# Kernel tuning notes

Measured on AMD Instinct MI355X. Metric: run time of the kernel, lower is better.

Reference implementation:

```python
import jax, jax.numpy as jnp
import numpy as np

NUM_HEADS = 8
NUM_GROUPS = 8
NUM_ITERATIONS = 3
DT = 0.1
EPS = 1e-5


def group_norm(x, scale, bias):
    # x: [B, C, H, W], GroupNorm(8, C)
    B, C, H, W = x.shape
    xg = x.reshape(B, NUM_GROUPS, C // NUM_GROUPS, H, W)
    mean = xg.mean(axis=(2, 3, 4), keepdims=True)
    var = xg.var(axis=(2, 3, 4), keepdims=True)
    xg = (xg - mean) * jax.lax.rsqrt(var + EPS)
    x = xg.reshape(B, C, H, W)
    return x * scale[None, :, None, None] + bias[None, :, None, None]


def setup_inputs() -> dict:
    key = jax.random.key(0)
    ks = jax.random.split(key, 4)
    B, C, H, W = 8, 512, 32, 32
    x = jax.random.normal(ks[0], (B, C, H, W), dtype=jnp.float32)
    qkv_w = jax.random.normal(ks[1], (3 * C, C), dtype=jnp.float32) * (1.0 / np.sqrt(C))
    proj_w = jax.random.normal(ks[2], (C, C), dtype=jnp.float32) * (1.0 / np.sqrt(C))
    inl_w = jax.random.normal(ks[3], (C, C), dtype=jnp.float32) * (1.0 / np.sqrt(C))
    return {
        "x": x,
        "gn_scale": jnp.ones((C,), jnp.float32),
        "gn_bias": jnp.zeros((C,), jnp.float32),
        "qkv_w": qkv_w,
        "qkv_b": jnp.zeros((3 * C,), jnp.float32),
        "proj_w": proj_w,
        "proj_b": jnp.zeros((C,), jnp.float32),
        "inl_w": inl_w,
        "inl_b": jnp.zeros((C,), jnp.float32),
    }


def reference(x, gn_scale, gn_bias, qkv_w, qkv_b, proj_w, proj_b, inl_w, inl_b):
    B, C, H, W = x.shape
    nh = NUM_HEADS
    hd = C // nh
    S = H * W

    h = group_norm(x, gn_scale, gn_bias)

    # 1x1 conv == channel matmul
    qkv = jnp.einsum('oc,bchw->bohw', qkv_w, h) + qkv_b[None, :, None, None]
    q, k, v = jnp.split(qkv, 3, axis=1)  # each [B, C, H, W]

    def to_heads(t):  # [B, C, H, W] -> [B, nh, S, hd]
        return t.reshape(B, nh, hd, S).transpose(0, 1, 3, 2)

    q, k, v = to_heads(q), to_heads(k), to_heads(v)

    scale = hd ** (-0.5)
    attn = jax.nn.softmax(jnp.einsum('bnsd,bntd->bnst', q, k) * scale, axis=-1)
    h = jnp.einsum('bnst,bntd->bnsd', attn, v)  # [B, nh, S, hd]

    # back to [B, S, C] for INL refinement
    h_flat = h.transpose(0, 1, 3, 2).reshape(B, C, S).transpose(0, 2, 1)

    # SimpleINLDynamics: iterative Euler refinement x <- x + dt * tanh(W x + b)
    def step(hf, _):
        hf = hf + DT * jnp.tanh(jnp.einsum('bsc,oc->bso', hf, inl_w) + inl_b)
        return hf, None
    h_flat, _ = jax.lax.scan(step, h_flat, None, length=NUM_ITERATIONS)

    h = h_flat.transpose(0, 2, 1).reshape(B, C, H, W)
    h = jnp.einsum('oc,bchw->bohw', proj_w, h) + proj_b[None, :, None, None]
    return x + h
```

## Files before the change

### kernel.cpp

```cpp
#include <hip/hip_runtime.h>
#include <math.h>

#define B_ 8
#define C_ 512
#define S_ 1024
#define HD 64
#define NHEADS 8
#define NGROUPS 8
#define DT_STEP 0.1f
#define EPS_GN 1e-5f
#define LOG2E 1.4426950408889634f

typedef __attribute__((ext_vector_type(8))) short bf16x8;
typedef __attribute__((ext_vector_type(4))) float f32x4;
typedef __attribute__((ext_vector_type(8))) unsigned short ushort8;
typedef __attribute__((ext_vector_type(4))) unsigned short ushort4_t;

static __device__ __forceinline__ unsigned short f2bf(float f) {
  unsigned int u = __builtin_bit_cast(unsigned int, f);
  u += 0x7fff + ((u >> 16) & 1);
  return (unsigned short)(u >> 16);
}

static __device__ __forceinline__ unsigned short f2bf_fast(float f) {
  unsigned int u = __builtin_bit_cast(unsigned int, f);
  return (unsigned short)((u + 0x8000u) >> 16);
}

static __device__ __forceinline__ float bf2f(unsigned short u) {
  unsigned int t = ((unsigned int)u) << 16;
  return __builtin_bit_cast(float, t);
}

static __device__ __forceinline__ float exp2_raw(float x) {
  return __builtin_amdgcn_exp2f(x);
}

static __device__ __forceinline__ float fast_tanh(float x) {
  float xc = fminf(fmaxf(x, -15.f), 15.f);
  float e = exp2_raw(xc * (2.0f * LOG2E));
  return (e - 1.f) / (e + 1.f);
}

__global__ __launch_bounds__(256) void prep_kernel(
    const float* __restrict__ a, const float* __restrict__ b, const float* __restrict__ c,
    unsigned short* __restrict__ A, unsigned short* __restrict__ B, unsigned short* __restrict__ C,
    const float* __restrict__ x, float* __restrict__ gpart) {
  int bid = blockIdx.x;
  int tid = threadIdx.x;
  if (bid < 384) {
    int off = bid * 2048;
    int i = off + tid * 8;
    f32x4 v0 = *(const f32x4*)(a + i);
    f32x4 v1 = *(const f32x4*)(a + i + 4);
    ushort8 o;
    o[0] = f2bf(v0[0]); o[1] = f2bf(v0[1]); o[2] = f2bf(v0[2]); o[3] = f2bf(v0[3]);
    o[4] = f2bf(v1[0]); o[5] = f2bf(v1[1]); o[6] = f2bf(v1[2]); o[7] = f2bf(v1[3]);
    *(ushort8*)(A + i) = o;
    return;
  }
  if (bid < 640) {
    const float* src; unsigned short* dst; int off;
    if (bid < 512) { src = b; dst = B; off = (bid - 384) * 2048; }
    else { src = c; dst = C; off = (bid - 512) * 2048; }
    int i = off + tid * 8;
    f32x4 v0 = *(const f32x4*)(src + i);
    f32x4 v1 = *(const f32x4*)(src + i + 4);
    ushort8 o;
    o[0] = f2bf(v0[0]); o[1] = f2bf(v0[1]); o[2] = f2bf(v0[2]); o[3] = f2bf(v0[3]);
    o[4] = f2bf(v1[0]); o[5] = f2bf(v1[1]); o[6] = f2bf(v1[2]); o[7] = f2bf(v1[3]);
    int orow = i >> 9, cbase = i & 511;
    int dsti = (cbase >> 5) * 16384 + orow * 32 + (cbase & 31);
    *(ushort8*)(dst + dsti) = o;
    return;
  }
  int sbid = bid - 640;
  int bg = sbid >> 3, chunk = sbid & 7;
  const float* xp = x + (size_t)bg * 65536 + (size_t)chunk * 8192;
  float sum = 0.f, sq = 0.f;
  #pragma unroll
  for (int i = 0; i < 8; ++i) {
    f32x4 v = *(const f32x4*)(xp + i * 1024 + tid * 4);
    sum += v[0] + v[1] + v[2] + v[3];
    sq += v[0]*v[0] + v[1]*v[1] + v[2]*v[2] + v[3]*v[3];
  }
  #pragma unroll
  for (int off = 32; off >= 1; off >>= 1) {
    sum += __shfl_xor(sum, off, 64);
    sq  += __shfl_xor(sq, off, 64);
  }
  __shared__ float s1[4], s2[4];
  int wave = tid >> 6, lane = tid & 63;
  if (lane == 0) { s1[wave] = sum; s2[wave] = sq; }
  __syncthreads();
  if (tid == 0) {
    float S = s1[0] + s1[1] + s1[2] + s1[3];
    float Q = s2[0] + s2[1] + s2[2] + s2[3];
    gpart[bg * 16 + chunk * 2] = S;
    gpart[bg * 16 + chunk * 2 + 1] = Q;
  }
}

__global__ __launch_bounds__(256) void gn_apply_t(
    const float* __restrict__ x, const float* __restrict__ gpart,
    const float* __restrict__ scale, const float* __restrict__ bias,
    unsigned short* __restrict__ h_t) {
  int bid = blockIdx.x;
  int bg = bid >> 4, st = bid & 15;
  int b = bg >> 3, g = bg & 7;
  float S = 0.f, Q = 0.f;
  #pragma unroll
  for (int i = 0; i < 8; ++i) {
    S += gpart[bg * 16 + i * 2];
    Q += gpart[bg * 16 + i * 2 + 1];
  }
  float mean = S / 65536.f;
  float var = Q / 65536.f - mean * mean;
  float inv = rsqrtf(var + EPS_GN);

  int tid = threadIdx.x;
  int sl = tid >> 2;
  int cq = (tid & 3) * 16;
  float sA[16], sB[16];
  #pragma unroll
  for (int u = 0; u < 16; ++u) {
    float scv = scale[g * 64 + cq + u];
    sA[u] = inv * scv;
    sB[u] = bias[g * 64 + cq + u] - mean * inv * scv;
  }

  const float* xp = x + ((size_t)b * C_ + (size_t)g * 64) * S_;
  __shared__ float tile[64][65];
  #pragma unroll
  for (int it = 0; it < 16; ++it) {
    int lin = it * 256 + tid;
    int c = lin >> 6, s = lin & 63;
    tile[c][s] = xp[(size_t)c * S_ + st * 64 + s];
  }
  __syncthreads();
  unsigned short vals[16];
  #pragma unroll
  for (int u = 0; u < 16; ++u)
    vals[u] = f2bf_fast(tile[cq + u][sl] * sA[u] + sB[u]);
  unsigned short* dst = h_t + ((size_t)b * S_ + st * 64 + sl) * C_ + g * 64 + cq;
  ushort8 lo, hi;
  #pragma unroll
  for (int u = 0; u < 8; ++u) { lo[u] = vals[u]; hi[u] = vals[u + 8]; }
  *(ushort8*)dst = lo;
  *(ushort8*)(dst + 8) = hi;
}

template<int MB, int NB, int WMG, int WNG>
__device__ __forceinline__ void gemm_nt_core(
    const unsigned short* __restrict__ Ab,
    const unsigned short* __restrict__ Bb,
    unsigned short* ldsA, unsigned short* ldsB,
    f32x4* acc) {
  constexpr int TI = (MB / WMG) / 16;
  constexpr int TJ = (NB / WNG) / 16;
  constexpr int NQA = MB * 4 / 256;
  constexpr int NQB = NB * 4 / 256;
  const int K = 512;
  const int tid = threadIdx.x;
  const int w = tid >> 6, lane = tid & 63, quad = lane >> 4, l15 = lane & 15;
  const int wm = (WNG == 1) ? w : ((WMG == 1) ? 0 : (w >> 1));
  const int wn = (WNG == 1) ? 0 : ((WMG == 1) ? w : (w & 1));

  ushort8 apf[NQA], bpf[NQB];
  #pragma unroll
  for (int q = 0; q < NQA; ++q) {
    int c = q * 256 + tid;
    apf[q] = *(const ushort8*)(Ab + (size_t)(c >> 2) * K + (c & 3) * 8);
  }
  #pragma unroll
  for (int q = 0; q < NQB; ++q) {
    int c = q * 256 + tid;
    bpf[q] = *(const ushort8*)(Bb + (size_t)(c >> 2) * K + (c & 3) * 8);
  }

  for (int k0 = 0; k0 < K; k0 += 32) {
    __syncthreads();
    #pragma unroll
    for (int q = 0; q < NQA; ++q) {
      int c = q * 256 + tid;
      *(ushort8*)(ldsA + c * 8) = apf[q];
    }
    #pragma unroll
    for (int q = 0; q < NQB; ++q) {
      int c = q * 256 + tid;
      *(ushort8*)(ldsB + c * 8) = bpf[q];
    }
    __syncthreads();
    if (k0 + 32 < K) {
      #pragma unroll
      for (int q = 0; q < NQA; ++q) {
        int c = q * 256 + tid;
        apf[q] = *(const ushort8*)(Ab + (size_t)(c >> 2) * K + k0 + 32 + (c & 3) * 8);
      }
      #pragma unroll
      for (int q = 0; q < NQB; ++q) {
        int c = q * 256 + tid;
        bpf[q] = *(const ushort8*)(Bb + (size_t)(c >> 2) * K + k0 + 32 + (c & 3) * 8);
      }
    }
    bf16x8 af[TI], bfr[TJ];
    #pragma unroll
    for (int i = 0; i < TI; ++i)
      af[i] = *(const bf16x8*)(ldsA + (wm * (MB / WMG) + i * 16 + l15) * 32 + quad * 8);
    #pragma unroll
    for (int j = 0; j < TJ; ++j)
      bfr[j] = *(const bf16x8*)(ldsB + (wn * (NB / WNG) + j * 16 + l15) * 32 + quad * 8);
    #pragma unroll
    for (int i = 0; i < TI; ++i)
      #pragma unroll
      for (int j = 0; j < TJ; ++j)
        acc[i * TJ + j] = __builtin_amdgcn_mfma_f32_16x16x32_bf16(af[i], bfr[j], acc[i * TJ + j], 0, 0, 0);
  }
}

__global__ __launch_bounds__(256) void gemm_qkv_mfma(
    const unsigned short* __restrict__ Wbf, const unsigned short* __restrict__ h_t,
    const float* __restrict__ bias,
    unsigned short* __restrict__ Qt, unsigned short* __restrict__ Kt,
    unsigned short* __restrict__ Vt) {
  __shared__ __align__(16) unsigned short ldsA[128 * 32];
  __shared__ __align__(16) unsigned short ldsB[128 * 32];
  int b = blockIdx.z;
  int bm = blockIdx.y * 128, bn = blockIdx.x * 128;
  f32x4 acc[16];
  #pragma unroll
  for (int t = 0; t < 16; ++t) acc[t] = (f32x4){0.f, 0.f, 0.f, 0.f};
  gemm_nt_core<128, 128, 2, 2>(Wbf + (size_t)bm * 512,
                               h_t + ((size_t)b * S_ + bn) * 512, ldsA, ldsB, acc);
  int tid = threadIdx.x, w = tid >> 6, lane = tid & 63, quad = lane >> 4, l15 = lane & 15;
  int wm = w >> 1, wn = w & 1;
  int tensor = bm >> 9;
  float qscale = (tensor == 0) ? 0.125f * LOG2E : 1.0f;
  #pragma unroll
  for (int i = 0; i < 4; ++i) {
    #pragma unroll
    for (int j = 0; j < 4; ++j) {
      int m0 = bm + wm * 64 + i * 16 + quad * 4;
      int ng = bn + wn * 64 + j * 16 + l15;
      f32x4 v = acc[i * 4 + j];
      if (tensor < 2) {
        int head = (m0 >> 6) & 7, d0 = m0 & 63;
        ushort4_t pk;
        #pragma unroll
        for (int r = 0; r < 4; ++r) pk[r] = f2bf((v[r] + bias[m0 + r]) * qscale);
        unsigned short* dst = (tensor ? Kt : Qt) +
            (((size_t)(b * 8 + head) * S_ + ng) * 64 + d0);
        *(ushort4_t*)dst = pk;
      } else {
        #pragma unroll
        for (int r = 0; r < 4; ++r)
          Vt[(size_t)b * (C_ * S_) + (size_t)(m0 - 1024 + r) * S_ + ng] = f2bf(v[r] + bias[m0 + r]);
      }
    }
  }
}

__global__ __launch_bounds__(256) void attn_mfma(
    const unsigned short* __restrict__ Qt,
    const unsigned short* __restrict__ Kt,
    const unsigned short* __restrict__ Vt,
    unsigned short* __restrict__ hflat_bf) {
  int tid = threadIdx.x, wave = tid >> 6, lane = tid & 63;
  int quad = lane >> 4, l15 = lane & 15;
  int bid = blockIdx.x;
  int bn = bid & 63, sblk = bid >> 6, b = bn >> 3, n = bn & 7;
  int s0w = sblk * 128 + wave * 32;

  __shared__ unsigned short k_lds[64][72];
  __shared__ unsigned short v_lds[64][72];
  __shared__ unsigned short p_lds[4][2][16][72];

  const unsigned short* Kb = Kt + ((size_t)(b * 8 + n)) * S_ * 64;
  const unsigned short* Vb = Vt + ((size_t)b * C_ + n * 64) * S_;

  bf16x8 qa[2][2];
  #pragma unroll
  for (int g = 0; g < 2; ++g) {
    const unsigned short* Qb = Qt + (((size_t)(b * 8 + n)) * S_ + s0w + g * 16 + l15) * 64;
    qa[g][0] = *(const bf16x8*)(Qb + quad * 8);
    qa[g][1] = *(const bf16x8*)(Qb + 32 + quad * 8);
  }

  bf16x8 ones;
  #pragma unroll
  for (int j = 0; j < 8; ++j) ones[j] = (short)0x3F80;

  f32x4 o_acc[2][4];
  f32x4 l_acc[2];
  #pragma unroll
  for (int g = 0; g < 2; ++g) {
    l_acc[g] = (f32x4){0.f, 0.f, 0.f, 0.f};
    #pragma unroll
    for (int dc = 0; dc < 4; ++dc) o_acc[g][dc] = (f32x4){0.f, 0.f, 0.f, 0.f};
  }

  int row0 = tid >> 3, c80 = (tid & 7) * 8;
  int row1 = (tid + 256) >> 3, c81 = c80;

  ushort8 kreg[2], vreg[2];
  kreg[0] = *(const ushort8*)(Kb + (size_t)row0 * 64 + c80);
  kreg[1] = *(const ushort8*)(Kb + (size_t)row1 * 64 + c81);
  vreg[0] = *(const ushort8*)(Vb + (size_t)row0 * S_ + c80);
  vreg[1] = *(const ushort8*)(Vb + (size_t)row1 * S_ + c81);

  for (int t0 = 0; t0 < S_; t0 += 64) {
    __syncthreads();
    *(ushort8*)&k_lds[row0][c80] = kreg[0];
    *(ushort8*)&k_lds[row1][c81] = kreg[1];
    *(ushort8*)&v_lds[row0][c80] = vreg[0];
    *(ushort8*)&v_lds[row1][c81] = vreg[1];
    __syncthreads();
    if (t0 + 64 < S_) {
      int t1 = t0 + 64;
      kreg[0] = *(const ushort8*)(Kb + (size_t)(t1 + row0) * 64 + c80);
      kreg[1] = *(const ushort8*)(Kb + (size_t)(t1 + row1) * 64 + c81);
      vreg[0] = *(const ushort8*)(Vb + (size_t)row0 * S_ + t1 + c80);
      vreg[1] = *(const ushort8*)(Vb + (size_t)row1 * S_ + t1 + c81);
    }

    f32x4 sc[2][4];
    #pragma unroll
    for (int tc = 0; tc < 4; ++tc) {
      bf16x8 kb0 = *(const bf16x8*)&k_lds[tc * 16 + l15][quad * 8];
      bf16x8 kb1 = *(const bf16x8*)&k_lds[tc * 16 + l15][32 + quad * 8];
      #pragma unroll
      for (int g = 0; g < 2; ++g) {
        f32x4 c = {0.f, 0.f, 0.f, 0.f};
        c = __builtin_amdgcn_mfma_f32_16x16x32_bf16(kb0, qa[g][0], c, 0, 0, 0);
        sc[g][tc] = __builtin_amdgcn_mfma_f32_16x16x32_bf16(kb1, qa[g][1], c, 0, 0, 0);
      }
    }

    #pragma unroll
    for (int g = 0; g < 2; ++g)
      #pragma unroll
      for (int tc = 0; tc < 4; ++tc) {
        ushort4_t p4;
        #pragma unroll
        for (int r = 0; r < 4; ++r) p4[r] = f2bf_fast(exp2_raw(sc[g][tc][r]));
        *(ushort4_t*)&p_lds[wave][g][l15][tc * 16 + quad * 4] = p4;
      }

    bf16x8 pa[2][2];
    #pragma unroll
    for (int g = 0; g < 2; ++g) {
      pa[g][0] = *(const bf16x8*)&p_lds[wave][g][l15][quad * 8];
      pa[g][1] = *(const bf16x8*)&p_lds[wave][g][l15][32 + quad * 8];
      l_acc[g] = __builtin_amdgcn_mfma_f32_16x16x32_bf16(pa[g][0], ones, l_acc[g], 0, 0, 0);
      l_acc[g] = __builtin_amdgcn_mfma_f32_16x16x32_bf16(pa[g][1], ones, l_acc[g], 0, 0, 0);
    }
    #pragma unroll
    for (int dc = 0; dc < 4; ++dc) {
      bf16x8 vb0 = *(const bf16x8*)&v_lds[dc * 16 + l15][quad * 8];
      bf16x8 vb1 = *(const bf16x8*)&v_lds[dc * 16 + l15][32 + quad * 8];
      #pragma unroll
      for (int g = 0; g < 2; ++g) {
        o_acc[g][dc] = __builtin_amdgcn_mfma_f32_16x16x32_bf16(pa[g][0], vb0, o_acc[g][dc], 0, 0, 0);
        o_acc[g][dc] = __builtin_amdgcn_mfma_f32_16x16x32_bf16(pa[g][1], vb1, o_acc[g][dc], 0, 0, 0);
      }
    }
  }

  #pragma unroll
  for (int g = 0; g < 2; ++g) {
    float inv_l[4];
    #pragma unroll
    for (int r = 0; r < 4; ++r) inv_l[r] = 1.f / l_acc[g][r];
    #pragma unroll
    for (int dc = 0; dc < 4; ++dc) {
      #pragma unroll
      for (int r = 0; r < 4; ++r) {
        int s = s0w + g * 16 + quad * 4 + r;
        size_t idx = ((size_t)b * S_ + s) * C_ + n * 64 + dc * 16 + l15;
        hflat_bf[idx] = f2bf_fast(o_acc[g][dc][r] * inv_l[r]);
      }
    }
  }
}

__global__ __launch_bounds__(1024, 4) void inl_proj_chain(
    const unsigned short* __restrict__ hbf,
    const unsigned short* __restrict__ Wi2,
    const unsigned short* __restrict__ Wp2,
    const float* __restrict__ ib, const float* __restrict__ pb,
    const float* __restrict__ x, float* __restrict__ Out) {
  __shared__ __align__(16) unsigned short h_lds[32][520];

  int tid = threadIdx.x;
  int wave = tid >> 6, lane = tid & 63, quad = lane >> 4, l15 = lane & 15;
  int wo = wave * 32;
  int bid = blockIdx.x;
  int b = bid >> 5, s0 = (bid & 31) * 32;

  const unsigned short* hsrc = hbf + (size_t)bid * 16384;
  ushort8 hv0 = *(const ushort8*)(hsrc + (size_t)tid * 8);
  ushort8 hv1 = *(const ushort8*)(hsrc + (size_t)(1024 + tid) * 8);

  const int wrow = (wo + l15) * 32 + quad * 8;

#define PREF_(na, nb, s) { \
    const unsigned short* wp_ = (((s) < 48) ? Wi2 : Wp2) + ((s) & 15) * 16384 + wrow; \
    na = *(const bf16x8*)(wp_); \
    nb = *(const bf16x8*)(wp_ + 512); }

  bf16x8 q0a, q0b, q1a, q1b, q2a, q2b, q3a, q3b;
  PREF_(q0a, q0b, 0); PREF_(q1a, q1b, 1); PREF_(q2a, q2b, 2); PREF_(q3a, q3b, 3);

  float bi0 = ib[wo + l15], bi1 = ib[wo + 16 + l15];
  float bp0 = pb[wo + l15], bp1 = pb[wo + 16 + l15];

  *(ushort8*)&h_lds[tid >> 6][(tid & 63) * 8] = hv0;
  { int lin = 1024 + tid; *(ushort8*)&h_lds[lin >> 6][(lin & 63) * 8] = hv1; }

  f32x4 acc00 = {0.f,0.f,0.f,0.f}, acc01 = {0.f,0.f,0.f,0.f};
  f32x4 acc10 = {0.f,0.f,0.f,0.f}, acc11 = {0.f,0.f,0.f,0.f};

  __syncthreads();

#define DOSLAB_(na, nb, s) { \
    bf16x8 a0_ = *(const bf16x8*)&h_lds[l15][((s) & 15) * 32 + quad * 8]; \
    bf16x8 a1_ = *(const bf16x8*)&h_lds[16 + l15][((s) & 15) * 32 + quad * 8]; \
    acc00 = __builtin_amdgcn_mfma_f32_16x16x32_bf16(a0_, na, acc00, 0, 0, 0); \
    acc10 = __builtin_amdgcn_mfma_f32_16x16x32_bf16(a1_, na, acc10, 0, 0, 0); \
    acc01 = __builtin_amdgcn_mfma_f32_16x16x32_bf16(a0_, nb, acc01, 0, 0, 0); \
    acc11 = __builtin_amdgcn_mfma_f32_16x16x32_bf16(a1_, nb, acc11, 0, 0, 0); }

#define STEP4_(s) \
    DOSLAB_(q0a, q0b, (s));     if ((s) + 4 < 64) PREF_(q0a, q0b, (s) + 4); \
    DOSLAB_(q1a, q1b, (s) + 1); if ((s) + 5 < 64) PREF_(q1a, q1b, (s) + 5); \
    DOSLAB_(q2a, q2b, (s) + 2); if ((s) + 6 < 64) PREF_(q2a, q2b, (s) + 6); \
    DOSLAB_(q3a, q3b, (s) + 3); if ((s) + 7 < 64) PREF_(q3a, q3b, (s) + 7);

#define UPDATE_ { \
    __syncthreads(); \
    _Pragma("unroll") \
    for (int r = 0; r < 4; ++r) { \
      int sa = quad * 4 + r, sb = 16 + quad * 4 + r; \
      int o0 = wo + l15, o1 = wo + 16 + l15; \
      h_lds[sa][o0] = f2bf_fast(bf2f(h_lds[sa][o0]) + DT_STEP * fast_tanh(acc00[r] + bi0)); \
      h_lds[sa][o1] = f2bf_fast(bf2f(h_lds[sa][o1]) + DT_STEP * fast_tanh(acc01[r] + bi1)); \
      h_lds[sb][o0] = f2bf_fast(bf2f(h_lds[sb][o0]) + DT_STEP * fast_tanh(acc10[r] + bi0)); \
      h_lds[sb][o1] = f2bf_fast(bf2f(h_lds[sb][o1]) + DT_STEP * fast_tanh(acc11[r] + bi1)); \
    } \
    acc00 = (f32x4){0.f,0.f,0.f,0.f}; acc01 = (f32x4){0.f,0.f,0.f,0.f}; \
    acc10 = (f32x4){0.f,0.f,0.f,0.f}; acc11 = (f32x4){0.f,0.f,0.f,0.f}; \
    __syncthreads(); }

  STEP4_(0); STEP4_(4); STEP4_(8); STEP4_(12);
  UPDATE_;
  STEP4_(16); STEP4_(20); STEP4_(24); STEP4_(28);
  UPDATE_;
  STEP4_(32); STEP4_(36); STEP4_(40); STEP4_(44);
  UPDATE_;
  STEP4_(48); STEP4_(52); STEP4_(56); STEP4_(60);

  {
    int o0 = wo + l15, o1 = wo + 16 + l15;
    size_t base0 = (((size_t)b * 512 + o0) << 10) + (size_t)(s0 + quad * 4);
    size_t base1 = (((size_t)b * 512 + o1) << 10) + (size_t)(s0 + quad * 4);
    f32x4 xv, ov;
    xv = *(const f32x4*)(x + base0);
    #pragma unroll
    for (int r = 0; r < 4; ++r) ov[r] = xv[r] + bp0 + acc00[r];
    *(f32x4*)(Out + base0) = ov;
    xv = *(const f32x4*)(x + base0 + 16);
    #pragma unroll
    for (int r = 0; r < 4; ++r) ov[r] = xv[r] + bp0 + acc10[r];
    *(f32x4*)(Out + base0 + 16) = ov;
    xv = *(const f32x4*)(x + base1);
    #pragma unroll
    for (int r = 0; r < 4; ++r) ov[r] = xv[r] + bp1 + acc01[r];
    *(f32x4*)(Out + base1) = ov;
    xv = *(const f32x4*)(x + base1 + 16);
    #pragma unroll
    for (int r = 0; r < 4; ++r) ov[r] = xv[r] + bp1 + acc11[r];
    *(f32x4*)(Out + base1 + 16) = ov;
  }
#undef PREF_
#undef DOSLAB_
#undef STEP4_
#undef UPDATE_
}

extern "C" void kernel_launch(void* const* d_in, const int* in_sizes, int n_in,
                              void* d_out, int out_size, void* d_ws, size_t ws_size,
                              hipStream_t stream) {
  const float* x        = (const float*)d_in[0];
  const float* gn_scale = (const float*)d_in[1];
  const float* gn_bias  = (const float*)d_in[2];
  const float* qkv_w    = (const float*)d_in[3];
  const float* qkv_b    = (const float*)d_in[4];
  const float* proj_w   = (const float*)d_in[5];
  const float* proj_b   = (const float*)d_in[6];
  const float* inl_w    = (const float*)d_in[7];
  const float* inl_b    = (const float*)d_in[8];
  float* out = (float*)d_out;
  float* ws = (float*)d_ws;

  unsigned short* Qt  = (unsigned short*)(ws + 8388608);
  unsigned short* Kt  = (unsigned short*)(ws + 10485760);
  unsigned short* Vt  = (unsigned short*)(ws + 12582912);
  unsigned short* h_t = (unsigned short*)(ws + 14680064);
  unsigned short* Abf = (unsigned short*)(ws + 16777216);
  float* gpart = ws + 18874368;
  unsigned short* qkvw_bf  = (unsigned short*)(ws + 18878464);
  unsigned short* inlw_bf  = qkvw_bf + 786432;
  unsigned short* projw_bf = inlw_bf + 262144;

  prep_kernel<<<1152, 256, 0, stream>>>(qkv_w, inl_w, proj_w, qkvw_bf, inlw_bf, projw_bf, x, gpart);
  gn_apply_t<<<1024, 256, 0, stream>>>(x, gpart, gn_scale, gn_bias, h_t);
  gemm_qkv_mfma<<<dim3(8, 12, 8), 256, 0, stream>>>(qkvw_bf, h_t, qkv_b, Qt, Kt, Vt);
  attn_mfma<<<512, 256, 0, stream>>>(Qt, Kt, Vt, Abf);
  inl_proj_chain<<<256, 1024, 0, stream>>>(Abf, inlw_bf, projw_bf, inl_b, proj_b, x, out);
}
```

Before: 184.3 us.

## Stage INL/proj weight slabs through LDS with register double-buffered prefetch

Each wave used to read its weight fragments for the INL and projection matmuls straight from global memory. Now the block cooperatively loads 64-column k-slabs of the weights into a new 72 KB LDS tile, prefetching the next slab into registers while computing the current one. This replaces per-wave scattered global loads with coalesced loads and LDS reads. The cost is two barriers per slab and much higher LDS use, which likely cuts occupancy for the 1024-thread blocks.

```diff
diff --git a/kernel.cpp b/kernel.cpp
--- a/kernel.cpp
+++ b/kernel.cpp
@@ -390,6 +390,7 @@
     const float* __restrict__ ib, const float* __restrict__ pb,
     const float* __restrict__ x, float* __restrict__ Out) {
   __shared__ __align__(16) unsigned short h_lds[32][520];
+  __shared__ __align__(16) unsigned short w_lds[512][72];
 
   int tid = threadIdx.x;
   int wave = tid >> 6, lane = tid & 63, quad = lane >> 4, l15 = lane & 15;
@@ -401,66 +402,71 @@
   ushort8 hv0 = *(const ushort8*)(hsrc + (size_t)tid * 8);
   ushort8 hv1 = *(const ushort8*)(hsrc + (size_t)(1024 + tid) * 8);
 
-  const int wrow = (wo + l15) * 32 + quad * 8;
-
-#define PREF_(na, nb, s) { \
-    const unsigned short* wp_ = (((s) < 48) ? Wi2 : Wp2) + ((s) & 15) * 16384 + wrow; \
-    na = *(const bf16x8*)(wp_); \
-    nb = *(const bf16x8*)(wp_ + 512); }
-
-  bf16x8 q0a, q0b, q1a, q1b, q2a, q2b, q3a, q3b;
-  PREF_(q0a, q0b, 0); PREF_(q1a, q1b, 1); PREF_(q2a, q2b, 2); PREF_(q3a, q3b, 3);
-
   float bi0 = ib[wo + l15], bi1 = ib[wo + 16 + l15];
   float bp0 = pb[wo + l15], bp1 = pb[wo + 16 + l15];
 
+  const int sr = tid >> 2, sc = (tid & 3) * 8;
+  ushort8 st0, st1, st2, st3;
+
+#define LDW_(g) { \
+    const unsigned short* p_ = (((g) < 24) ? Wi2 : Wp2) + ((g) & 7) * 32768; \
+    st0 = *(const ushort8*)(p_ + (size_t)tid * 8); \
+    st1 = *(const ushort8*)(p_ + (size_t)(1024 + tid) * 8); \
+    st2 = *(const ushort8*)(p_ + (size_t)(2048 + tid) * 8); \
+    st3 = *(const ushort8*)(p_ + (size_t)(3072 + tid) * 8); }
+
+#define STW_ { \
+    *(ushort8*)&w_lds[sr][sc]            = st0; \
+    *(ushort8*)&w_lds[256 + sr][sc]      = st1; \
+    *(ushort8*)&w_lds[sr][32 + sc]       = st2; \
+    *(ushort8*)&w_lds[256 + sr][32 + sc] = st3; }
+
+  LDW_(0);
+
   *(ushort8*)&h_lds[tid >> 6][(tid & 63) * 8] = hv0;
   { int lin = 1024 + tid; *(ushort8*)&h_lds[lin >> 6][(lin & 63) * 8] = hv1; }
 
   f32x4 acc00 = {0.f,0.f,0.f,0.f}, acc01 = {0.f,0.f,0.f,0.f};
   f32x4 acc10 = {0.f,0.f,0.f,0.f}, acc11 = {0.f,0.f,0.f,0.f};
 
-  __syncthreads();
-
-#define DOSLAB_(na, nb, s) { \
-    bf16x8 a0_ = *(const bf16x8*)&h_lds[l15][((s) & 15) * 32 + quad * 8]; \
-    bf16x8 a1_ = *(const bf16x8*)&h_lds[16 + l15][((s) & 15) * 32 + quad * 8]; \
-    acc00 = __builtin_amdgcn_mfma_f32_16x16x32_bf16(a0_, na, acc00, 0, 0, 0); \
-    acc10 = __builtin_amdgcn_mfma_f32_16x16x32_bf16(a1_, na, acc10, 0, 0, 0); \
-    acc01 = __builtin_amdgcn_mfma_f32_16x16x32_bf16(a0_, nb, acc01, 0, 0, 0); \
-    acc11 = __builtin_amdgcn_mfma_f32_16x16x32_bf16(a1_, nb, acc11, 0, 0, 0); }
-
-#define STEP4_(s) \
-    DOSLAB_(q0a, q0b, (s));     if ((s) + 4 < 64) PREF_(q0a, q0b, (s) + 4); \
-    DOSLAB_(q1a, q1b, (s) + 1); if ((s) + 5 < 64) PREF_(q1a, q1b, (s) + 5); \
-    DOSLAB_(q2a, q2b, (s) + 2); if ((s) + 6 < 64) PREF_(q2a, q2b, (s) + 6); \
-    DOSLAB_(q3a, q3b, (s) + 3); if ((s) + 7 < 64) PREF_(q3a, q3b, (s) + 7);
-
-#define UPDATE_ { \
-    __syncthreads(); \
-    _Pragma("unroll") \
-    for (int r = 0; r < 4; ++r) { \
-      int sa = quad * 4 + r, sb = 16 + quad * 4 + r; \
-      int o0 = wo + l15, o1 = wo + 16 + l15; \
-      h_lds[sa][o0] = f2bf_fast(bf2f(h_lds[sa][o0]) + DT_STEP * fast_tanh(acc00[r] + bi0)); \
-      h_lds[sa][o1] = f2bf_fast(bf2f(h_lds[sa][o1]) + DT_STEP * fast_tanh(acc01[r] + bi1)); \
-      h_lds[sb][o0] = f2bf_fast(bf2f(h_lds[sb][o0]) + DT_STEP * fast_tanh(acc10[r] + bi0)); \
-      h_lds[sb][o1] = f2bf_fast(bf2f(h_lds[sb][o1]) + DT_STEP * fast_tanh(acc11[r] + bi1)); \
-    } \
-    acc00 = (f32x4){0.f,0.f,0.f,0.f}; acc01 = (f32x4){0.f,0.f,0.f,0.f}; \
-    acc10 = (f32x4){0.f,0.f,0.f,0.f}; acc11 = (f32x4){0.f,0.f,0.f,0.f}; \
-    __syncthreads(); }
-
-  STEP4_(0); STEP4_(4); STEP4_(8); STEP4_(12);
-  UPDATE_;
-  STEP4_(16); STEP4_(20); STEP4_(24); STEP4_(28);
-  UPDATE_;
-  STEP4_(32); STEP4_(36); STEP4_(40); STEP4_(44);
-  UPDATE_;
-  STEP4_(48); STEP4_(52); STEP4_(56); STEP4_(60);
+  const int o0 = wo + l15, o1 = wo + 16 + l15;
+
+  for (int g = 0; g < 32; ++g) {
+    __syncthreads();
+    STW_;
+    __syncthreads();
+    if (g + 1 < 32) LDW_(g + 1);
+
+    int kb = (g & 7) * 64 + quad * 8;
+    #pragma unroll
+    for (int kh = 0; kh < 2; ++kh) {
+      bf16x8 a0 = *(const bf16x8*)&h_lds[l15][kb + kh * 32];
+      bf16x8 a1 = *(const bf16x8*)&h_lds[16 + l15][kb + kh * 32];
+      bf16x8 na = *(const bf16x8*)&w_lds[o0][kh * 32 + quad * 8];
+      bf16x8 nb = *(const bf16x8*)&w_lds[o1][kh * 32 + quad * 8];
+      acc00 = __builtin_amdgcn_mfma_f32_16x16x32_bf16(a0, na, acc00, 0, 0, 0);
+      acc10 = __builtin_amdgcn_mfma_f32_16x16x32_bf16(a1, na, acc10, 0, 0, 0);
+      acc01 = __builtin_amdgcn_mfma_f32_16x16x32_bf16(a0, nb, acc01, 0, 0, 0);
+      acc11 = __builtin_amdgcn_mfma_f32_16x16x32_bf16(a1, nb, acc11, 0, 0, 0);
+    }
+
+    if ((g & 7) == 7 && g < 31) {
+      __syncthreads();
+      #pragma unroll
+      for (int r = 0; r < 4; ++r) {
+        int sa = quad * 4 + r, sb = 16 + quad * 4 + r;
+        h_lds[sa][o0] = f2bf_fast(bf2f(h_lds[sa][o0]) + DT_STEP * fast_tanh(acc00[r] + bi0));
+        h_lds[sa][o1] = f2bf_fast(bf2f(h_lds[sa][o1]) + DT_STEP * fast_tanh(acc01[r] + bi1));
+        h_lds[sb][o0] = f2bf_fast(bf2f(h_lds[sb][o0]) + DT_STEP * fast_tanh(acc10[r] + bi0));
+        h_lds[sb][o1] = f2bf_fast(bf2f(h_lds[sb][o1]) + DT_STEP * fast_tanh(acc11[r] + bi1));
+      }
+      acc00 = (f32x4){0.f,0.f,0.f,0.f}; acc01 = (f32x4){0.f,0.f,0.f,0.f};
+      acc10 = (f32x4){0.f,0.f,0.f,0.f}; acc11 = (f32x4){0.f,0.f,0.f,0.f};
+      __syncthreads();
+    }
+  }
 
   {
-    int o0 = wo + l15, o1 = wo + 16 + l15;
     size_t base0 = (((size_t)b * 512 + o0) << 10) + (size_t)(s0 + quad * 4);
     size_t base1 = (((size_t)b * 512 + o1) << 10) + (size_t)(s0 + quad * 4);
     f32x4 xv, ov;
@@ -481,10 +487,8 @@
     for (int r = 0; r < 4; ++r) ov[r] = xv[r] + bp1 + acc11[r];
     *(f32x4*)(Out + base1 + 16) = ov;
   }
-#undef PREF_
-#undef DOSLAB_
-#undef STEP4_
-#undef UPDATE_
+#undef LDW_
+#undef STW_
 }
 
 extern "C" void kernel_launch(void* const* d_in, const int* in_sizes, int n_in,
```

New measurement: 197.4 us. +7.1%, slower.
